# Performance work log

Measured on AMD Instinct MI355X. Metric: run time of the kernel, lower is better.

## Reference

```python
import jax, jax.numpy as jnp
import numpy as np

NEG = -1e9
SLOPE = 0.2  # LeakyReLU slope (GAT convention)


def setup_inputs() -> dict:
    key = jax.random.key(0)
    ks = jax.random.split(key, 10)
    T, N, E, F, Hd = 32, 512, 64, 64, 64
    x = jax.random.normal(ks[0], (T, N, F), dtype=jnp.float32)
    # Hyperedge incidence [N, E]; guarantee every node is in >= 1 hyperedge.
    Hm = (jax.random.uniform(ks[1], (N, E)) < (2.0 / E)).astype(jnp.int32)
    Hm = Hm.at[jnp.arange(N), jnp.arange(N) % E].set(1)
    # Industry adjacency [N, N] with self loops.
    adj = (jax.random.uniform(ks[2], (N, N)) < 0.05).astype(jnp.int32)
    adj = adj.at[jnp.arange(N), jnp.arange(N)].set(1)
    sc = 0.1
    W = jax.random.normal(ks[3], (F, Hd), jnp.float32) * sc
    a_hyp = jax.random.normal(ks[4], (Hd,), jnp.float32) * sc
    a_ind = jax.random.normal(ks[5], (Hd,), jnp.float32) * sc
    Wc1 = jax.random.normal(ks[6], (Hd, Hd), jnp.float32) * sc
    bc1 = jnp.zeros((Hd,), jnp.float32)
    wc2 = jax.random.normal(ks[7], (Hd,), jnp.float32) * sc
    bc2 = jnp.zeros((), jnp.float32)
    return dict(x=x, H=Hm, adj=adj, nhid=Hd, W=W, a_hyp=a_hyp, a_ind=a_ind,
                Wc1=Wc1, bc1=bc1, wc2=wc2, bc2=bc2)


def _edgeconv(feats, mask, Wc1, bc1, wc2, bc2):
    """Attention pooling over the second-to-last (set) axis.
    feats: [..., K, Hd], mask: broadcastable to [..., K] (bool). -> [..., Hd]"""
    z = jnp.maximum(feats @ Wc1 + bc1, 0.0) @ wc2 + bc2  # [..., K]
    z = jnp.where(mask, z, NEG)
    alpha = jax.nn.softmax(z, axis=-1)
    return jnp.einsum('...k,...kd->...d', alpha, feats)


def reference(x, H, adj, nhid, W, a_hyp, a_ind, Wc1, bc1, wc2, bc2):
    # x: [T, N, F]; H: [N, E] incidence; adj: [N, N]. Eval mode: dropout = id.
    Hb = H.astype(bool)          # [N, E]
    Ab = adj.astype(bool)        # [N, N]
    h = x @ W                    # [T, N, Hd]

    # --- hyperedge_attn: intra-hyperedge node attention (GAT-style) ---
    s_hyp = jax.nn.leaky_relu(h @ a_hyp, SLOPE)                 # [T, N]
    logits = jnp.where(Hb[None, :, :], s_hyp[:, :, None], NEG)  # [T, N, E]
    alpha = jax.nn.softmax(logits, axis=1)                      # over nodes in edge
    # per-(edge,node) contribution; original layout [E,T,N,Hd] -> here [T,N,E,Hd]
    all_hyper = jax.nn.elu(alpha[..., None] * h[:, :, None, :])  # [T, N, E, Hd]

    # --- industry attention over adj ---
    s_ind = jax.nn.leaky_relu(h @ a_ind, SLOPE)                   # [T, N]
    li = jnp.where(Ab[None, :, :], s_ind[:, None, :], NEG)        # [T, N, N]
    beta = jax.nn.softmax(li, axis=-1)
    industry = jnp.einsum('tij,tjd->tid', beta, h)                # [T, N, Hd]

    # --- per-node loop, vectorized ---
    # y8: EdgeConv over the hyperedges containing each node (mask = H row).
    # When a node has exactly 1 hyperedge, masked softmax selects it exactly,
    # which reproduces the original else-branch.
    y8 = _edgeconv(all_hyper, Hb[None, :, :], Wc1, bc1, wc2, bc2)  # [T, N, Hd]
    pair = jnp.stack([industry, y8], axis=2)                       # [T, N, 2, Hd]
    y9 = _edgeconv(pair, jnp.ones((1, 1, 2), bool), Wc1, bc1, wc2, bc2)
    return y9                                                      # [T, N, Hd]
```

## Files before the change

kernel.cpp:

```cpp
#include <hip/hip_runtime.h>

#define T_DIM 32
#define N_DIM 512
#define E_DIM 64
#define F_DIM 64
#define HD    64

static_assert(E_DIM == 64 && HD == 64 && F_DIM == 64, "wave-mapped dims");

__device__ __forceinline__ float wave_sum(float v) {
    #pragma unroll
    for (int off = 32; off > 0; off >>= 1) v += __shfl_xor(v, off, 64);
    return v;
}
__device__ __forceinline__ float wave_max(float v) {
    #pragma unroll
    for (int off = 32; off > 0; off >>= 1) v = fmaxf(v, __shfl_xor(v, off, 64));
    return v;
}

#define K1_R 16
__global__ __launch_bounds__(256) void k1_h_s(
    const float* __restrict__ x, const float* __restrict__ W,
    const float* __restrict__ a_hyp, const float* __restrict__ a_ind,
    float* __restrict__ h, float* __restrict__ s_hyp, float* __restrict__ s_ind)
{
    __shared__ float xl[K1_R * F_DIM];
    const int wave = threadIdx.x >> 6;
    const int lane = threadIdx.x & 63;
    const int row0 = blockIdx.x * K1_R;

    ((float4*)xl)[threadIdx.x] = ((const float4*)(x + (size_t)row0 * F_DIM))[threadIdx.x];

    float wcol[F_DIM];
    #pragma unroll
    for (int f = 0; f < F_DIM; ++f) wcol[f] = W[f * HD + lane];
    const float ah = a_hyp[lane], ai = a_ind[lane];
    __syncthreads();

    #pragma unroll
    for (int r = wave; r < K1_R; r += 4) {
        float a0 = 0.f, a1 = 0.f, a2 = 0.f, a3 = 0.f;
        #pragma unroll
        for (int f = 0; f < F_DIM; f += 4) {
            const float4 xv = *(const float4*)&xl[r * F_DIM + f];
            a0 = fmaf(xv.x, wcol[f + 0], a0);
            a1 = fmaf(xv.y, wcol[f + 1], a1);
            a2 = fmaf(xv.z, wcol[f + 2], a2);
            a3 = fmaf(xv.w, wcol[f + 3], a3);
        }
        const float acc = (a0 + a1) + (a2 + a3);
        h[(size_t)(row0 + r) * HD + lane] = acc;
        const float sh = wave_sum(acc * ah);
        const float si = wave_sum(acc * ai);
        if (lane == 0) {
            s_hyp[row0 + r] = sh > 0.f ? sh : 0.2f * sh;
            s_ind[row0 + r] = si > 0.f ? si : 0.2f * si;
        }
    }
}

#define K2_BLOCKS (T_DIM * E_DIM / 4)
__global__ __launch_bounds__(256) void k23_stats_industry(
    const int* __restrict__ Hm, const int* __restrict__ adj,
    const float* __restrict__ s_hyp, const float* __restrict__ s_ind,
    const float* __restrict__ h,
    float* __restrict__ m_e, float* __restrict__ d_e,
    float* __restrict__ industry)
{
    const int wave = threadIdx.x >> 6;
    const int lane = threadIdx.x & 63;

    if (blockIdx.x < K2_BLOCKS) {
        const int idx = blockIdx.x * 4 + wave;
        const int t = idx >> 6;
        const int e = idx & 63;
        int   mem[N_DIM / 64];
        float sv [N_DIM / 64];
        float mx = -3.0e38f;
        #pragma unroll
        for (int c = 0; c < N_DIM / 64; ++c) {
            const int n = c * 64 + lane;
            mem[c] = Hm[n * E_DIM + e];
            sv [c] = s_hyp[t * N_DIM + n];
            if (mem[c]) mx = fmaxf(mx, sv[c]);
        }
        mx = wave_max(mx);
        float sum = 0.f;
        #pragma unroll
        for (int c = 0; c < N_DIM / 64; ++c)
            if (mem[c]) sum += expf(sv[c] - mx);
        sum = wave_sum(sum);
        if (lane == 0) { m_e[idx] = mx; d_e[idx] = sum; }
    } else {
        const int idx = (blockIdx.x - K2_BLOCKS) * 4 + wave;
        const int t = idx >> 9;
        const int i = idx & (N_DIM - 1);
        const int*   arow = adj + i * N_DIM;
        const float* srow = s_ind + t * N_DIM;
        int   mem[N_DIM / 64];
        float sv [N_DIM / 64];
        float mx = -3.0e38f;
        #pragma unroll
        for (int c = 0; c < N_DIM / 64; ++c) {
            const int j = c * 64 + lane;
            mem[c] = arow[j];
            sv [c] = srow[j];
            if (mem[c]) mx = fmaxf(mx, sv[c]);
        }
        mx = wave_max(mx);
        const float* hbase = h + (size_t)t * N_DIM * HD;
        float ac0 = 0.f, ac1 = 0.f, ac2 = 0.f, ac3 = 0.f, sum = 0.f;
        #pragma unroll
        for (int c = 0; c < N_DIM / 64; ++c) {
            const float ev = mem[c] ? expf(sv[c] - mx) : 0.f;
            sum += ev;
            unsigned long long mk = __ballot(mem[c] != 0);
            const int base = c * 64;
            while (mk) {
                const int b0 = __ffsll((long long)mk) - 1; mk &= mk - 1;
                const bool h1 = mk != 0;
                int b1 = 0; if (h1) { b1 = __ffsll((long long)mk) - 1; mk &= mk - 1; }
                const bool h2 = mk != 0;
                int b2 = 0; if (h2) { b2 = __ffsll((long long)mk) - 1; mk &= mk - 1; }
                const bool h3 = mk != 0;
                int b3 = 0; if (h3) { b3 = __ffsll((long long)mk) - 1; mk &= mk - 1; }
                const float v0 = hbase[(size_t)(base + b0) * HD + lane];
                const float v1 = hbase[(size_t)(base + b1) * HD + lane];
                const float v2 = hbase[(size_t)(base + b2) * HD + lane];
                const float v3 = hbase[(size_t)(base + b3) * HD + lane];
                const float w0 = __shfl(ev, b0, 64);
                const float w1 = h1 ? __shfl(ev, b1, 64) : 0.f;
                const float w2 = h2 ? __shfl(ev, b2, 64) : 0.f;
                const float w3 = h3 ? __shfl(ev, b3, 64) : 0.f;
                ac0 = fmaf(w0, v0, ac0);
                ac1 = fmaf(w1, v1, ac1);
                ac2 = fmaf(w2, v2, ac2);
                ac3 = fmaf(w3, v3, ac3);
            }
        }
        sum = wave_sum(sum);
        industry[(size_t)idx * HD + lane] = ((ac0 + ac1) + (ac2 + ac3)) / sum;
    }
}

__global__ __launch_bounds__(256) void k4_final(
    const int* __restrict__ Hm, const float* __restrict__ s_hyp,
    const float* __restrict__ m_e, const float* __restrict__ d_e,
    const float* __restrict__ h, const float* __restrict__ industry,
    const float* __restrict__ Wc1, const float* __restrict__ bc1,
    const float* __restrict__ wc2, const float* __restrict__ bc2,
    float* __restrict__ out)
{
    __shared__ float fl[4 * 2 * HD];
    const int wave = threadIdx.x >> 6;
    const int lane = threadIdx.x & 63;
    const int idx  = blockIdx.x * 4 + wave;
    const int t = idx >> 9;
    const int n = idx & (N_DIM - 1);
    float* fw = fl + wave * 2 * HD;

    float wreg[HD];
    #pragma unroll
    for (int d = 0; d < HD; ++d) wreg[d] = Wc1[d * HD + lane];
    const float bc1v = bc1[lane];
    const float wc2v = wc2[lane];
    const float bc2v = bc2[0];

    const float hv = h[(size_t)idx * HD + lane];
    const float sh = s_hyp[idx];

    const int memv = Hm[n * E_DIM + lane];
    float alpha_e = 0.f;
    if (memv)
        alpha_e = expf(sh - m_e[t * E_DIM + lane]) * __frcp_rn(d_e[t * E_DIM + lane]);
    unsigned long long mk = __ballot(memv != 0);

    float zmax = -3.0e38f, zsum = 0.f, acc = 0.f;
    while (mk) {
        const int e = __ffsll((long long)mk) - 1;
        mk &= mk - 1;
        const float a = __shfl(alpha_e, e, 64);
        float f = a * hv;
        f = f > 0.f ? f : expm1f(f);
        fw[lane] = f;
        float u0 = 0.f, u1 = 0.f, u2 = 0.f, u3 = 0.f;
        #pragma unroll
        for (int d = 0; d < HD; d += 4) {
            const float4 fv = *(const float4*)&fw[d];
            u0 = fmaf(fv.x, wreg[d + 0], u0);
            u1 = fmaf(fv.y, wreg[d + 1], u1);
            u2 = fmaf(fv.z, wreg[d + 2], u2);
            u3 = fmaf(fv.w, wreg[d + 3], u3);
        }
        const float u = (u0 + u1) + (u2 + u3);
        const float z = wave_sum(fmaxf(u + bc1v, 0.f) * wc2v) + bc2v;
        if (z > zmax) {
            const float sc = expf(zmax - z);
            acc *= sc; zsum *= sc; zmax = z;
        }
        const float w = expf(z - zmax);
        zsum += w;
        acc = fmaf(w, f, acc);
    }
    const float y8 = acc / zsum;

    const float indv = industry[(size_t)idx * HD + lane];
    fw[lane]      = indv;
    fw[HD + lane] = y8;
    float p0 = 0.f, p1 = 0.f, q0 = 0.f, q1 = 0.f;
    #pragma unroll
    for (int d = 0; d < HD; d += 4) {
        const float4 iv = *(const float4*)&fw[d];
        const float4 yv = *(const float4*)&fw[HD + d];
        p0 = fmaf(iv.x, wreg[d + 0], p0);
        p1 = fmaf(iv.y, wreg[d + 1], p1);
        p0 = fmaf(iv.z, wreg[d + 2], p0);
        p1 = fmaf(iv.w, wreg[d + 3], p1);
        q0 = fmaf(yv.x, wreg[d + 0], q0);
        q1 = fmaf(yv.y, wreg[d + 1], q1);
        q0 = fmaf(yv.z, wreg[d + 2], q0);
        q1 = fmaf(yv.w, wreg[d + 3], q1);
    }
    const float z0 = wave_sum(fmaxf(p0 + p1 + bc1v, 0.f) * wc2v) + bc2v;
    const float z1 = wave_sum(fmaxf(q0 + q1 + bc1v, 0.f) * wc2v) + bc2v;
    const float zm = fmaxf(z0, z1);
    const float w0 = expf(z0 - zm), w1 = expf(z1 - zm);
    out[(size_t)idx * HD + lane] = fmaf(w0, indv, w1 * y8) / (w0 + w1);
}

extern "C" void kernel_launch(void* const* d_in, const int* in_sizes, int n_in,
                              void* d_out, int out_size, void* d_ws, size_t ws_size,
                              hipStream_t stream) {
    const float* x     = (const float*)d_in[0];
    const int*   Hm    = (const int*)  d_in[1];
    const int*   adj   = (const int*)  d_in[2];
    const float* W     = (const float*)d_in[4];
    const float* a_hyp = (const float*)d_in[5];
    const float* a_ind = (const float*)d_in[6];
    const float* Wc1   = (const float*)d_in[7];
    const float* bc1   = (const float*)d_in[8];
    const float* wc2   = (const float*)d_in[9];
    const float* bc2   = (const float*)d_in[10];
    float* out = (float*)d_out;

    float* ws       = (float*)d_ws;
    float* h        = ws;
    float* s_hyp    = h + (size_t)T_DIM * N_DIM * HD;
    float* s_ind    = s_hyp + T_DIM * N_DIM;
    float* m_e      = s_ind + T_DIM * N_DIM;
    float* d_e      = m_e + T_DIM * E_DIM;
    float* industry = d_e + T_DIM * E_DIM;

    k1_h_s<<<T_DIM * N_DIM / K1_R, 256, 0, stream>>>(x, W, a_hyp, a_ind, h, s_hyp, s_ind);
    k23_stats_industry<<<K2_BLOCKS + T_DIM * N_DIM / 4, 256, 0, stream>>>(
        Hm, adj, s_hyp, s_ind, h, m_e, d_e, industry);
    k4_final<<<T_DIM * N_DIM / 4, 256, 0, stream>>>(Hm, s_hyp, m_e, d_e, h, industry,
                                                    Wc1, bc1, wc2, bc2, out);
}
```

Measured before the change: 141.5 us.

## Build CSR adjacency and transposed incidence, drop max-subtraction in softmaxes

The first kernel gains extra blocks that build a per-row CSR neighbor list of the adjacency (capped at 128 neighbors) and a transposed copy of the hyperedge incidence. The industry gather then walks only the compact neighbor lists instead of scanning all 512 adjacency ints per (t,i) wave, and the edge-stat pass reads the incidence coalesced. All softmaxes drop the running-max subtraction, which removes a reduction pass and the online rescaling. The EdgeConv loop now processes two hyperedges per iteration with paired wave reductions. The risks are overflow in expf without max-subtraction and silent truncation if any node has more than 128 neighbors, since the fixed cap is not checked.

```diff
diff --git a/kernel.cpp b/kernel.cpp
--- a/kernel.cpp
+++ b/kernel.cpp
@@ -5,6 +5,7 @@
 #define E_DIM 64
 #define F_DIM 64
 #define HD    64
+#define NBR_CAP 128
 
 static_assert(E_DIM == 64 && HD == 64 && F_DIM == 64, "wave-mapped dims");
 
@@ -13,140 +14,148 @@
     for (int off = 32; off > 0; off >>= 1) v += __shfl_xor(v, off, 64);
     return v;
 }
-__device__ __forceinline__ float wave_max(float v) {
-    #pragma unroll
-    for (int off = 32; off > 0; off >>= 1) v = fmaxf(v, __shfl_xor(v, off, 64));
-    return v;
+__device__ __forceinline__ void wave_sum2(float& a, float& b) {
+    #pragma unroll
+    for (int off = 32; off > 0; off >>= 1) {
+        a += __shfl_xor(a, off, 64);
+        b += __shfl_xor(b, off, 64);
+    }
 }
 
 #define K1_R 16
+#define K1_ROWBLK (T_DIM * N_DIM / K1_R)
+#define K1_CSRBLK (N_DIM / 4)
 __global__ __launch_bounds__(256) void k1_h_s(
     const float* __restrict__ x, const float* __restrict__ W,
     const float* __restrict__ a_hyp, const float* __restrict__ a_ind,
-    float* __restrict__ h, float* __restrict__ s_hyp, float* __restrict__ s_ind)
-{
-    __shared__ float xl[K1_R * F_DIM];
-    const int wave = threadIdx.x >> 6;
-    const int lane = threadIdx.x & 63;
-    const int row0 = blockIdx.x * K1_R;
-
-    ((float4*)xl)[threadIdx.x] = ((const float4*)(x + (size_t)row0 * F_DIM))[threadIdx.x];
-
-    float wcol[F_DIM];
-    #pragma unroll
-    for (int f = 0; f < F_DIM; ++f) wcol[f] = W[f * HD + lane];
-    const float ah = a_hyp[lane], ai = a_ind[lane];
-    __syncthreads();
-
-    #pragma unroll
-    for (int r = wave; r < K1_R; r += 4) {
-        float a0 = 0.f, a1 = 0.f, a2 = 0.f, a3 = 0.f;
-        #pragma unroll
-        for (int f = 0; f < F_DIM; f += 4) {
-            const float4 xv = *(const float4*)&xl[r * F_DIM + f];
-            a0 = fmaf(xv.x, wcol[f + 0], a0);
-            a1 = fmaf(xv.y, wcol[f + 1], a1);
-            a2 = fmaf(xv.z, wcol[f + 2], a2);
-            a3 = fmaf(xv.w, wcol[f + 3], a3);
-        }
-        const float acc = (a0 + a1) + (a2 + a3);
-        h[(size_t)(row0 + r) * HD + lane] = acc;
-        const float sh = wave_sum(acc * ah);
-        const float si = wave_sum(acc * ai);
-        if (lane == 0) {
-            s_hyp[row0 + r] = sh > 0.f ? sh : 0.2f * sh;
-            s_ind[row0 + r] = si > 0.f ? si : 0.2f * si;
-        }
-    }
-}
-
-#define K2_BLOCKS (T_DIM * E_DIM / 4)
-__global__ __launch_bounds__(256) void k23_stats_industry(
-    const int* __restrict__ Hm, const int* __restrict__ adj,
-    const float* __restrict__ s_hyp, const float* __restrict__ s_ind,
-    const float* __restrict__ h,
-    float* __restrict__ m_e, float* __restrict__ d_e,
-    float* __restrict__ industry)
+    const int* __restrict__ adj, const int* __restrict__ Hm,
+    float* __restrict__ h, float* __restrict__ s_hyp, float* __restrict__ s_ind,
+    int* __restrict__ degs, int* __restrict__ nbrs, int* __restrict__ Ht)
 {
     const int wave = threadIdx.x >> 6;
     const int lane = threadIdx.x & 63;
 
+    if (blockIdx.x < K1_ROWBLK) {
+        __shared__ float xl[K1_R * F_DIM];
+        const int row0 = blockIdx.x * K1_R;
+        ((float4*)xl)[threadIdx.x] =
+            ((const float4*)(x + (size_t)row0 * F_DIM))[threadIdx.x];
+        float wcol[F_DIM];
+        #pragma unroll
+        for (int f = 0; f < F_DIM; ++f) wcol[f] = W[f * HD + lane];
+        const float ah = a_hyp[lane], ai = a_ind[lane];
+        __syncthreads();
+        #pragma unroll
+        for (int r = wave; r < K1_R; r += 4) {
+            float a0 = 0.f, a1 = 0.f, a2 = 0.f, a3 = 0.f;
+            #pragma unroll
+            for (int f = 0; f < F_DIM; f += 4) {
+                const float4 xv = *(const float4*)&xl[r * F_DIM + f];
+                a0 = fmaf(xv.x, wcol[f + 0], a0);
+                a1 = fmaf(xv.y, wcol[f + 1], a1);
+                a2 = fmaf(xv.z, wcol[f + 2], a2);
+                a3 = fmaf(xv.w, wcol[f + 3], a3);
+            }
+            const float acc = (a0 + a1) + (a2 + a3);
+            h[(size_t)(row0 + r) * HD + lane] = acc;
+            float sh = acc * ah, si = acc * ai;
+            wave_sum2(sh, si);
+            if (lane == 0) {
+                s_hyp[row0 + r] = sh > 0.f ? sh : 0.2f * sh;
+                s_ind[row0 + r] = si > 0.f ? si : 0.2f * si;
+            }
+        }
+    } else if (blockIdx.x < K1_ROWBLK + K1_CSRBLK) {
+        const int i = (blockIdx.x - K1_ROWBLK) * 4 + wave;
+        int deg = 0;
+        #pragma unroll
+        for (int c = 0; c < N_DIM / 64; ++c) {
+            const int j = c * 64 + lane;
+            const bool bit = adj[(size_t)i * N_DIM + j] != 0;
+            const unsigned long long mask = __ballot(bit);
+            if (bit) {
+                const int pos = deg + __popcll(mask & ((1ull << lane) - 1ull));
+                nbrs[i * NBR_CAP + pos] = j;
+            }
+            deg += __popcll(mask);
+        }
+        if (lane == 0) degs[i] = deg;
+    } else {
+        for (int idx = threadIdx.x; idx < N_DIM * E_DIM; idx += 256) {
+            const int n = idx >> 6, e = idx & 63;
+            Ht[e * N_DIM + n] = Hm[idx];
+        }
+    }
+}
+
+#define K2_BLOCKS (T_DIM * E_DIM / 4)
+__global__ __launch_bounds__(256) void k23_stats_industry(
+    const int* __restrict__ Ht, const int* __restrict__ degs,
+    const int* __restrict__ nbrs,
+    const float* __restrict__ s_hyp, const float* __restrict__ s_ind,
+    const float* __restrict__ h,
+    float* __restrict__ d_e, float* __restrict__ industry)
+{
+    const int wave = threadIdx.x >> 6;
+    const int lane = threadIdx.x & 63;
+
     if (blockIdx.x < K2_BLOCKS) {
         const int idx = blockIdx.x * 4 + wave;
-        const int t = idx >> 6;
-        const int e = idx & 63;
-        int   mem[N_DIM / 64];
-        float sv [N_DIM / 64];
-        float mx = -3.0e38f;
+        const int t = idx >> 6, e = idx & 63;
+        const int*   hrow = Ht + e * N_DIM;
+        const float* srow = s_hyp + t * N_DIM;
+        float sum = 0.f;
         #pragma unroll
         for (int c = 0; c < N_DIM / 64; ++c) {
             const int n = c * 64 + lane;
-            mem[c] = Hm[n * E_DIM + e];
-            sv [c] = s_hyp[t * N_DIM + n];
-            if (mem[c]) mx = fmaxf(mx, sv[c]);
-        }
-        mx = wave_max(mx);
-        float sum = 0.f;
-        #pragma unroll
-        for (int c = 0; c < N_DIM / 64; ++c)
-            if (mem[c]) sum += expf(sv[c] - mx);
+            if (hrow[n]) sum += expf(srow[n]);
+        }
         sum = wave_sum(sum);
-        if (lane == 0) { m_e[idx] = mx; d_e[idx] = sum; }
+        if (lane == 0) d_e[idx] = sum;
     } else {
         const int idx = (blockIdx.x - K2_BLOCKS) * 4 + wave;
-        const int t = idx >> 9;
-        const int i = idx & (N_DIM - 1);
-        const int*   arow = adj + i * N_DIM;
-        const float* srow = s_ind + t * N_DIM;
-        int   mem[N_DIM / 64];
-        float sv [N_DIM / 64];
-        float mx = -3.0e38f;
-        #pragma unroll
-        for (int c = 0; c < N_DIM / 64; ++c) {
-            const int j = c * 64 + lane;
-            mem[c] = arow[j];
-            sv [c] = srow[j];
-            if (mem[c]) mx = fmaxf(mx, sv[c]);
-        }
-        mx = wave_max(mx);
+        const int t = idx >> 9, i = idx & (N_DIM - 1);
+        const int deg = degs[i];
+        const int* nb = nbrs + i * NBR_CAP;
+        const float* st = s_ind + t * N_DIM;
         const float* hbase = h + (size_t)t * N_DIM * HD;
-        float ac0 = 0.f, ac1 = 0.f, ac2 = 0.f, ac3 = 0.f, sum = 0.f;
-        #pragma unroll
-        for (int c = 0; c < N_DIM / 64; ++c) {
-            const float ev = mem[c] ? expf(sv[c] - mx) : 0.f;
-            sum += ev;
-            unsigned long long mk = __ballot(mem[c] != 0);
-            const int base = c * 64;
-            while (mk) {
-                const int b0 = __ffsll((long long)mk) - 1; mk &= mk - 1;
-                const bool h1 = mk != 0;
-                int b1 = 0; if (h1) { b1 = __ffsll((long long)mk) - 1; mk &= mk - 1; }
-                const bool h2 = mk != 0;
-                int b2 = 0; if (h2) { b2 = __ffsll((long long)mk) - 1; mk &= mk - 1; }
-                const bool h3 = mk != 0;
-                int b3 = 0; if (h3) { b3 = __ffsll((long long)mk) - 1; mk &= mk - 1; }
-                const float v0 = hbase[(size_t)(base + b0) * HD + lane];
-                const float v1 = hbase[(size_t)(base + b1) * HD + lane];
-                const float v2 = hbase[(size_t)(base + b2) * HD + lane];
-                const float v3 = hbase[(size_t)(base + b3) * HD + lane];
-                const float w0 = __shfl(ev, b0, 64);
-                const float w1 = h1 ? __shfl(ev, b1, 64) : 0.f;
-                const float w2 = h2 ? __shfl(ev, b2, 64) : 0.f;
-                const float w3 = h3 ? __shfl(ev, b3, 64) : 0.f;
+        float evp = 0.f, ac0 = 0.f, ac1 = 0.f, ac2 = 0.f, ac3 = 0.f;
+        for (int base = 0; base < deg; base += 64) {
+            const int k = base + lane;
+            const bool valid = k < deg;
+            const int j = valid ? nb[k] : 0;
+            const float ev = valid ? expf(st[j]) : 0.f;
+            evp += ev;
+            const int cnt = min(deg - base, 64);
+            int kk = 0;
+            for (; kk + 4 <= cnt; kk += 4) {
+                const int j0 = __shfl(j, kk, 64),     j1 = __shfl(j, kk + 1, 64);
+                const int j2 = __shfl(j, kk + 2, 64), j3 = __shfl(j, kk + 3, 64);
+                const float w0 = __shfl(ev, kk, 64),     w1 = __shfl(ev, kk + 1, 64);
+                const float w2 = __shfl(ev, kk + 2, 64), w3 = __shfl(ev, kk + 3, 64);
+                const float v0 = hbase[(size_t)j0 * HD + lane];
+                const float v1 = hbase[(size_t)j1 * HD + lane];
+                const float v2 = hbase[(size_t)j2 * HD + lane];
+                const float v3 = hbase[(size_t)j3 * HD + lane];
                 ac0 = fmaf(w0, v0, ac0);
                 ac1 = fmaf(w1, v1, ac1);
                 ac2 = fmaf(w2, v2, ac2);
                 ac3 = fmaf(w3, v3, ac3);
             }
-        }
-        sum = wave_sum(sum);
-        industry[(size_t)idx * HD + lane] = ((ac0 + ac1) + (ac2 + ac3)) / sum;
+            for (; kk < cnt; ++kk) {
+                const int jj = __shfl(j, kk, 64);
+                const float ww = __shfl(ev, kk, 64);
+                ac0 = fmaf(ww, hbase[(size_t)jj * HD + lane], ac0);
+            }
+        }
+        const float evsum = wave_sum(evp);
+        industry[(size_t)idx * HD + lane] = ((ac0 + ac1) + (ac2 + ac3)) / evsum;
     }
 }
 
 __global__ __launch_bounds__(256) void k4_final(
     const int* __restrict__ Hm, const float* __restrict__ s_hyp,
-    const float* __restrict__ m_e, const float* __restrict__ d_e,
+    const float* __restrict__ d_e,
     const float* __restrict__ h, const float* __restrict__ industry,
     const float* __restrict__ Wc1, const float* __restrict__ bc1,
     const float* __restrict__ wc2, const float* __restrict__ bc2,
@@ -156,8 +165,7 @@
     const int wave = threadIdx.x >> 6;
     const int lane = threadIdx.x & 63;
     const int idx  = blockIdx.x * 4 + wave;
-    const int t = idx >> 9;
-    const int n = idx & (N_DIM - 1);
+    const int t = idx >> 9, n = idx & (N_DIM - 1);
     float* fw = fl + wave * 2 * HD;
 
     float wreg[HD];
@@ -168,40 +176,47 @@
     const float bc2v = bc2[0];
 
     const float hv = h[(size_t)idx * HD + lane];
-    const float sh = s_hyp[idx];
+    const float esh = expf(s_hyp[idx]);
 
     const int memv = Hm[n * E_DIM + lane];
-    float alpha_e = 0.f;
-    if (memv)
-        alpha_e = expf(sh - m_e[t * E_DIM + lane]) * __frcp_rn(d_e[t * E_DIM + lane]);
+    const float alpha = memv ? esh * __frcp_rn(d_e[t * E_DIM + lane]) : 0.f;
     unsigned long long mk = __ballot(memv != 0);
 
-    float zmax = -3.0e38f, zsum = 0.f, acc = 0.f;
+    float zsum = 0.f, acc = 0.f;
     while (mk) {
-        const int e = __ffsll((long long)mk) - 1;
-        mk &= mk - 1;
-        const float a = __shfl(alpha_e, e, 64);
-        float f = a * hv;
-        f = f > 0.f ? f : expm1f(f);
-        fw[lane] = f;
+        const int e0 = __ffsll((long long)mk) - 1; mk &= mk - 1;
+        const bool have1 = mk != 0;
+        const int e1 = have1 ? __ffsll((long long)mk) - 1 : e0;
+        if (have1) mk &= mk - 1;
+        const float a0 = __shfl(alpha, e0, 64);
+        const float a1 = __shfl(alpha, e1, 64);
+        float f0 = a0 * hv; f0 = f0 > 0.f ? f0 : expm1f(f0);
+        float f1 = a1 * hv; f1 = f1 > 0.f ? f1 : expm1f(f1);
+        fw[lane]      = f0;
+        fw[HD + lane] = f1;
         float u0 = 0.f, u1 = 0.f, u2 = 0.f, u3 = 0.f;
+        float v0 = 0.f, v1 = 0.f, v2 = 0.f, v3 = 0.f;
         #pragma unroll
         for (int d = 0; d < HD; d += 4) {
-            const float4 fv = *(const float4*)&fw[d];
-            u0 = fmaf(fv.x, wreg[d + 0], u0);
-            u1 = fmaf(fv.y, wreg[d + 1], u1);
-            u2 = fmaf(fv.z, wreg[d + 2], u2);
-            u3 = fmaf(fv.w, wreg[d + 3], u3);
-        }
-        const float u = (u0 + u1) + (u2 + u3);
-        const float z = wave_sum(fmaxf(u + bc1v, 0.f) * wc2v) + bc2v;
-        if (z > zmax) {
-            const float sc = expf(zmax - z);
-            acc *= sc; zsum *= sc; zmax = z;
-        }
-        const float w = expf(z - zmax);
-        zsum += w;
-        acc = fmaf(w, f, acc);
+            const float4 A = *(const float4*)&fw[d];
+            const float4 B = *(const float4*)&fw[HD + d];
+            u0 = fmaf(A.x, wreg[d + 0], u0);
+            u1 = fmaf(A.y, wreg[d + 1], u1);
+            u2 = fmaf(A.z, wreg[d + 2], u2);
+            u3 = fmaf(A.w, wreg[d + 3], u3);
+            v0 = fmaf(B.x, wreg[d + 0], v0);
+            v1 = fmaf(B.y, wreg[d + 1], v1);
+            v2 = fmaf(B.z, wreg[d + 2], v2);
+            v3 = fmaf(B.w, wreg[d + 3], v3);
+        }
+        float p = fmaxf((u0 + u1) + (u2 + u3) + bc1v, 0.f) * wc2v;
+        float q = fmaxf((v0 + v1) + (v2 + v3) + bc1v, 0.f) * wc2v;
+        wave_sum2(p, q);
+        const float w0 = expf(p + bc2v);
+        const float w1 = have1 ? expf(q + bc2v) : 0.f;
+        zsum += w0 + w1;
+        acc = fmaf(w0, f0, acc);
+        acc = fmaf(w1, f1, acc);
     }
     const float y8 = acc / zsum;
 
@@ -222,10 +237,10 @@
         q0 = fmaf(yv.z, wreg[d + 2], q0);
         q1 = fmaf(yv.w, wreg[d + 3], q1);
     }
-    const float z0 = wave_sum(fmaxf(p0 + p1 + bc1v, 0.f) * wc2v) + bc2v;
-    const float z1 = wave_sum(fmaxf(q0 + q1 + bc1v, 0.f) * wc2v) + bc2v;
-    const float zm = fmaxf(z0, z1);
-    const float w0 = expf(z0 - zm), w1 = expf(z1 - zm);
+    float zp = fmaxf(p0 + p1 + bc1v, 0.f) * wc2v;
+    float zq = fmaxf(q0 + q1 + bc1v, 0.f) * wc2v;
+    wave_sum2(zp, zq);
+    const float w0 = expf(zp + bc2v), w1 = expf(zq + bc2v);
     out[(size_t)idx * HD + lane] = fmaf(w0, indv, w1 * y8) / (w0 + w1);
 }
 
@@ -248,13 +263,16 @@
     float* h        = ws;
     float* s_hyp    = h + (size_t)T_DIM * N_DIM * HD;
     float* s_ind    = s_hyp + T_DIM * N_DIM;
-    float* m_e      = s_ind + T_DIM * N_DIM;
-    float* d_e      = m_e + T_DIM * E_DIM;
+    float* d_e      = s_ind + T_DIM * N_DIM;
     float* industry = d_e + T_DIM * E_DIM;
-
-    k1_h_s<<<T_DIM * N_DIM / K1_R, 256, 0, stream>>>(x, W, a_hyp, a_ind, h, s_hyp, s_ind);
+    int*   degs     = (int*)(industry + (size_t)T_DIM * N_DIM * HD);
+    int*   nbrs     = degs + N_DIM;
+    int*   Ht       = nbrs + N_DIM * NBR_CAP;
+
+    k1_h_s<<<K1_ROWBLK + K1_CSRBLK + 1, 256, 0, stream>>>(
+        x, W, a_hyp, a_ind, adj, Hm, h, s_hyp, s_ind, degs, nbrs, Ht);
     k23_stats_industry<<<K2_BLOCKS + T_DIM * N_DIM / 4, 256, 0, stream>>>(
-        Hm, adj, s_hyp, s_ind, h, m_e, d_e, industry);
-    k4_final<<<T_DIM * N_DIM / 4, 256, 0, stream>>>(Hm, s_hyp, m_e, d_e, h, industry,
-                                                    Wc1, bc1, wc2, bc2, out);
-}
+        Ht, degs, nbrs, s_hyp, s_ind, h, d_e, industry);
+    k4_final<<<T_DIM * N_DIM / 4, 256, 0, stream>>>(
+        Hm, s_hyp, d_e, h, industry, Wc1, bc1, wc2, bc2, out);
+}
```

Result: slower. 164.3 us (+16.1%).
